# Performance work log

Measured on AMD Instinct MI355X. Metric: run time of the kernel, lower is better.

The kernel has to match this reference:

```python
import jax, jax.numpy as jnp
import numpy as np

NUM_HEADS = 16
D_MODEL = 1024
B, T = 2, 2048


def setup_inputs() -> dict:
    key = jax.random.key(0)
    ks = jax.random.split(key, 5)
    s = 1.0 / np.sqrt(D_MODEL)
    return {
        "x": jax.random.normal(ks[0], (B, T, D_MODEL), dtype=jnp.float32),
        "Wq": jax.random.normal(ks[1], (D_MODEL, D_MODEL), dtype=jnp.float32) * s,
        "Wk": jax.random.normal(ks[2], (D_MODEL, D_MODEL), dtype=jnp.float32) * s,
        "Wv": jax.random.normal(ks[3], (D_MODEL, D_MODEL), dtype=jnp.float32) * s,
        "Wo": jax.random.normal(ks[4], (D_MODEL, D_MODEL), dtype=jnp.float32) * s,
    }


def reference(x, Wq, Wk, Wv, Wo):
    # x: [B, T, D]; W*: [D, D] (torch nn.Linear weight layout, y = x @ W.T)
    b, t, d = x.shape
    h = NUM_HEADS
    hd = d // h

    def split_heads(y):
        # [B, T, D] -> [B, H, T, hd]
        return y.reshape(b, t, h, hd).transpose(0, 2, 1, 3)

    q = split_heads(x @ Wq.T)
    k = split_heads(x @ Wk.T)
    v = split_heads(x @ Wv.T)

    # scale uses last dim AFTER head split: 1/sqrt(head_dim)
    scores = jnp.einsum("bhqd,bhkd->bhqk", q, k) / jnp.sqrt(jnp.asarray(hd, x.dtype))
    causal = jnp.tril(jnp.ones((t, t), dtype=bool))  # [T, T]
    scores = jnp.where(causal[None, None], scores, -jnp.inf)
    attn = jax.nn.softmax(scores, axis=-1)  # [B, H, T, T]

    out = jnp.einsum("bhqk,bhkd->bhqd", attn, v)  # [B, H, T, hd]
    out = out.transpose(0, 2, 1, 3).reshape(b, t, d)  # concat heads
    return out @ Wo.T
```

## Files before the change

### kernel.cpp

```cpp
#include <hip/hip_runtime.h>
#include <hip/hip_bf16.h>

#define T_SEQ 2048
#define DM    1024
#define MTOT  4096

typedef short v8s __attribute__((ext_vector_type(8)));
typedef short v4s __attribute__((ext_vector_type(4)));
typedef float v4f __attribute__((ext_vector_type(4)));

__device__ __forceinline__ unsigned short f2bf(float f) {
  union { float f; unsigned int u; } x; x.f = f;
  return (unsigned short)((x.u + (((x.u >> 16) & 1u) + 0x7fffu)) >> 16);
}

__device__ __forceinline__ unsigned int pk2(float a, float b) {
  unsigned int ua = __float_as_uint(a) + 0x8000u;
  unsigned int ub = __float_as_uint(b) + 0x8000u;
  return __builtin_amdgcn_perm(ub, ua, 0x07060302u);
}

__device__ __forceinline__ v8s pack8bf(v4f a, v4f b) {
  union { v8s s; unsigned int u[4]; } o;
  o.u[0] = pk2(a[0], a[1]);
  o.u[1] = pk2(a[2], a[3]);
  o.u[2] = pk2(b[0], b[1]);
  o.u[3] = pk2(b[2], b[3]);
  return o.s;
}

__device__ __forceinline__ float fast_exp2(float x) {
#if __has_builtin(__builtin_amdgcn_exp2f)
  return __builtin_amdgcn_exp2f(x);
#else
  return exp2f(x);
#endif
}

__device__ __forceinline__ void gload16(const void* g, void* lds) {
  __builtin_amdgcn_global_load_lds(
      (const __attribute__((address_space(1))) unsigned int*)g,
      (__attribute__((address_space(3))) unsigned int*)lds, 16, 0, 0);
}

__global__ __launch_bounds__(256) void convert_all(
    const float* __restrict__ x,
    const float* __restrict__ Wq, const float* __restrict__ Wk,
    const float* __restrict__ Wv, const float* __restrict__ Wo,
    unsigned short* __restrict__ xb, unsigned short* __restrict__ wb)
{
  int i = blockIdx.x * 256 + threadIdx.x;
  const float4* src;
  ushort4* dst;
  int idx;
  if (i < (1 << 20)) {
    src = (const float4*)x; dst = (ushort4*)xb; idx = i;
  } else {
    int j = i - (1 << 20);
    int wsel = j >> 18;
    idx = j & ((1 << 18) - 1);
    const float* s = (wsel == 0) ? Wq : (wsel == 1) ? Wk : (wsel == 2) ? Wv : Wo;
    src = (const float4*)s;
    dst = (ushort4*)(wb + (size_t)wsel * DM * DM);
  }
  float4 v = src[idx];
  ushort4 o = { f2bf(v.x), f2bf(v.y), f2bf(v.z), f2bf(v.w) };
  dst[idx] = o;
}

__global__ __launch_bounds__(256) void qkv_fused2(
    const unsigned short* __restrict__ xb,
    const unsigned short* __restrict__ wb,
    unsigned short* __restrict__ Qw, unsigned short* __restrict__ Kw,
    unsigned short* __restrict__ Vtw)
{
  __shared__ unsigned short smem[20480];
  unsigned short* As = smem;

  const int tid  = threadIdx.x;
  const int wv   = tid >> 6, l = tid & 63;
  const int lrow = l & 15, lq = l >> 4;
  const int wm = wv >> 1;
  const int wn = wv & 1;
  const int srow = l >> 3, sslot = l & 7;
  const int swz  = sslot ^ (srow & 7);
  const int m0 = blockIdx.x * 128, n0 = blockIdx.y * 64;

  v4f acc[3][4][2];
#pragma unroll
  for (int z = 0; z < 3; ++z)
#pragma unroll
    for (int mt = 0; mt < 4; ++mt)
#pragma unroll
      for (int nt = 0; nt < 2; ++nt) acc[z][mt][nt] = (v4f){0.f, 0.f, 0.f, 0.f};

  const size_t aBase = (size_t)(m0 + wv * 32 + srow) * DM + swz * 8;
  const size_t bBase = (size_t)(n0 + wv * 16 + srow) * DM + swz * 8;

  for (int k0 = 0; k0 < DM; k0 += 64) {
    __syncthreads();
#pragma unroll
    for (int i = 0; i < 4; ++i)
      gload16(xb + aBase + (size_t)i * 8 * DM + k0, As + (wv * 32 + i * 8) * 64);
#pragma unroll
    for (int z = 0; z < 3; ++z)
#pragma unroll
      for (int i = 0; i < 2; ++i)
        gload16(wb + (size_t)z * DM * DM + bBase + (size_t)i * 8 * DM + k0,
                smem + 8192 + z * 4096 + (wv * 16 + i * 8) * 64);
    __syncthreads();
#pragma unroll
    for (int kc = 0; kc < 2; ++kc) {
      const int aslot = ((kc << 2) | lq) ^ (lrow & 7);
      v8s af[4];
#pragma unroll
      for (int mt = 0; mt < 4; ++mt)
        af[mt] = *(const v8s*)&As[(wm * 64 + mt * 16 + lrow) * 64 + aslot * 8];
#pragma unroll
      for (int z = 0; z < 3; ++z) {
        const unsigned short* Bz = smem + 8192 + z * 4096;
        v8s bf[2];
#pragma unroll
        for (int nt = 0; nt < 2; ++nt)
          bf[nt] = *(const v8s*)&Bz[(wn * 32 + nt * 16 + lrow) * 64 + aslot * 8];
#pragma unroll
        for (int mt = 0; mt < 4; ++mt)
#pragma unroll
          for (int nt = 0; nt < 2; ++nt)
            acc[z][mt][nt] = __builtin_amdgcn_mfma_f32_16x16x32_bf16(
                af[mt], bf[nt], acc[z][mt][nt], 0, 0, 0);
      }
    }
  }

#pragma unroll
  for (int z = 0; z < 2; ++z) {
    unsigned short* Y = z ? Kw : Qw;
#pragma unroll
    for (int mt = 0; mt < 4; ++mt)
#pragma unroll
      for (int nt = 0; nt < 2; ++nt)
#pragma unroll
        for (int r = 0; r < 4; ++r) {
          int row = m0 + wm * 64 + mt * 16 + lq * 4 + r;
          int col = n0 + wn * 32 + nt * 16 + lrow;
          Y[(size_t)row * DM + col] = f2bf(acc[z][mt][nt][r]);
        }
  }

  __syncthreads();
#pragma unroll
  for (int mt = 0; mt < 4; ++mt)
#pragma unroll
    for (int nt = 0; nt < 2; ++nt)
#pragma unroll
      for (int r = 0; r < 4; ++r) {
        int trow = wm * 64 + mt * 16 + lq * 4 + r;
        int col  = wn * 32 + nt * 16 + lrow;
        int slot = (col >> 3) ^ (trow & 7);
        smem[trow * 64 + slot * 8 + (col & 7)] = f2bf(acc[2][mt][nt][r]);
      }
  __syncthreads();
  {
    const int d = tid & 63;
    const int quarter = tid >> 6;
    const int bb = m0 >> 11;
    const int tblk = (m0 & 2047) >> 7;
    const int h = n0 >> 6;
    const int bh = bb * 16 + h;
    unsigned short* dst = Vtw + (((size_t)bh * 16 + tblk) * 64 + d) * 128;
    const int ch = d >> 3, e7 = d & 7;
#pragma unroll
    for (int jj = 0; jj < 4; ++jj) {
      unsigned short vals[8];
#pragma unroll
      for (int e = 0; e < 8; ++e) {
        int st = quarter * 32 + (e >> 2) * 16 + jj * 4 + (e & 3);
        vals[e] = smem[st * 64 + (ch ^ (st & 7)) * 8 + e7];
      }
      *(v8s*)(dst + (quarter * 4 + jj) * 8) = *(const v8s*)vals;
    }
  }
}

__global__ __launch_bounds__(256) void oproj_gemm2(
    const unsigned short* __restrict__ AO,
    const unsigned short* __restrict__ Wob,
    float* __restrict__ Y)
{
  __shared__ unsigned short smem[12288];
  unsigned short* As = smem;
  unsigned short* Bs = smem + 4096;

  const int tid  = threadIdx.x;
  const int wv   = tid >> 6, l = tid & 63;
  const int lrow = l & 15, lq = l >> 4;
  const int wm = wv >> 1;
  const int wn = wv & 1;
  const int srow = l >> 3, sslot = l & 7;
  const int swz  = sslot ^ (srow & 7);
  const int m0 = blockIdx.x * 64, n0 = blockIdx.y * 128;

  v4f acc[2][4];
#pragma unroll
  for (int mt = 0; mt < 2; ++mt)
#pragma unroll
    for (int nt = 0; nt < 4; ++nt) acc[mt][nt] = (v4f){0.f, 0.f, 0.f, 0.f};

  const size_t aBase = (size_t)(m0 + wv * 16 + srow) * DM + swz * 8;
  const size_t bBase = (size_t)(n0 + wv * 32 + srow) * DM + swz * 8;

  for (int k0 = 0; k0 < DM; k0 += 64) {
    __syncthreads();
#pragma unroll
    for (int i = 0; i < 2; ++i)
      gload16(AO + aBase + (size_t)i * 8 * DM + k0, As + (wv * 16 + i * 8) * 64);
#pragma unroll
    for (int i = 0; i < 4; ++i)
      gload16(Wob + bBase + (size_t)i * 8 * DM + k0, Bs + (wv * 32 + i * 8) * 64);
    __syncthreads();
#pragma unroll
    for (int kc = 0; kc < 2; ++kc) {
      const int aslot = ((kc << 2) | lq) ^ (lrow & 7);
      v8s af[2], bf[4];
#pragma unroll
      for (int mt = 0; mt < 2; ++mt)
        af[mt] = *(const v8s*)&As[(wm * 32 + mt * 16 + lrow) * 64 + aslot * 8];
#pragma unroll
      for (int nt = 0; nt < 4; ++nt)
        bf[nt] = *(const v8s*)&Bs[(wn * 64 + nt * 16 + lrow) * 64 + aslot * 8];
#pragma unroll
      for (int mt = 0; mt < 2; ++mt)
#pragma unroll
        for (int nt = 0; nt < 4; ++nt)
          acc[mt][nt] = __builtin_amdgcn_mfma_f32_16x16x32_bf16(
              af[mt], bf[nt], acc[mt][nt], 0, 0, 0);
    }
  }
#pragma unroll
  for (int mt = 0; mt < 2; ++mt)
#pragma unroll
    for (int nt = 0; nt < 4; ++nt)
#pragma unroll
      for (int r = 0; r < 4; ++r) {
        int row = m0 + wm * 32 + mt * 16 + lq * 4 + r;
        int col = n0 + wn * 64 + nt * 16 + lrow;
        Y[(size_t)row * DM + col] = acc[mt][nt][r];
      }
}

__global__ __launch_bounds__(256) void attn8(
    const unsigned short* __restrict__ Q,
    const unsigned short* __restrict__ K,
    const unsigned short* __restrict__ Vt,
    unsigned short* __restrict__ O)
{
  __shared__ unsigned short Ks[2][128 * 64];
  __shared__ unsigned short Vts[2][64 * 128];

  const int tid  = threadIdx.x;
  const int wave = tid >> 6;
  const int lane = tid & 63;
  const int lrow = lane & 15;
  const int lq   = lane >> 4;
  const int gid  = blockIdx.x;
  const int qt   = 31 - (gid >> 5);
  const int bh   = gid & 31;
  const int b = bh >> 4, h = bh & 15;

  union { v8s s; unsigned int u[4]; } ones;
  ones.u[0] = 0x3F803F80u; ones.u[1] = 0x3F803F80u;
  ones.u[2] = 0x3F803F80u; ones.u[3] = 0x3F803F80u;

  const int qrow = qt * 64 + wave * 16 + lrow;
  const unsigned short* qp = Q + ((size_t)(b * T_SEQ + qrow)) * DM + h * 64;
  v8s qf0 = *(const v8s*)(qp + lq * 8);
  v8s qf1 = *(const v8s*)(qp + 32 + lq * 8);

  v4f oacc[4];
#pragma unroll
  for (int dt = 0; dt < 4; ++dt) oacc[dt] = (v4f){0.f, 0.f, 0.f, 0.f};
  v4f sacc = {0.f, 0.f, 0.f, 0.f};

  const int n128 = (qt >> 1) + 1;

  const int kchunk = (lane & 7) ^ ((lane >> 3) & 7);
  const unsigned short* kg =
      K + ((size_t)(b * T_SEQ) + wave * 8 + (lane >> 3)) * DM + h * 64 + kchunk * 8;
  const int vd = wave * 4 + (lane >> 4);
  const int vslot = lane & 15;
  const int vchunk = (vslot & 8) | ((vslot & 7) ^ (vd & 7));
  const unsigned short* vg =
      Vt + ((size_t)bh * 1024 + vd) * 128 + vchunk * 8;

  const int slot0 = lq ^ (lrow & 7);
  const int slot1 = (4 + lq) ^ (lrow & 7);

#define STAGE(tt, buf) do {                                                   \
    unsigned short* kd_ = Ks[buf] + (wave * 8) * 64;                          \
    _Pragma("unroll")                                                         \
    for (int i_ = 0; i_ < 4; ++i_)                                            \
      gload16(kg + ((size_t)(tt) * 128 + i_ * 32) * DM, kd_ + i_ * 32 * 64);  \
    unsigned short* vd_ = Vts[buf] + (wave * 4) * 128;                        \
    _Pragma("unroll")                                                         \
    for (int i_ = 0; i_ < 4; ++i_)                                            \
      gload16(vg + (size_t)(tt) * 8192 + i_ * 2048, vd_ + i_ * 16 * 128);     \
  } while (0)

  STAGE(0, 0);
  __syncthreads();

  int cur = 0;
  for (int tt = 0; tt < n128; ++tt) {
    if (tt + 1 < n128) STAGE(tt + 1, cur ^ 1);

    const int kb = tt * 128;
    const unsigned short* Kss = Ks[cur];
    const unsigned short* Vss = Vts[cur];

    v4f s[8];
    __builtin_amdgcn_s_setprio(1);
#pragma unroll
    for (int nt = 0; nt < 8; ++nt) {
      v4f a = {0.f, 0.f, 0.f, 0.f};
      v8s k0 = *(const v8s*)&Kss[(nt * 16 + lrow) * 64 + slot0 * 8];
      a = __builtin_amdgcn_mfma_f32_16x16x32_bf16(k0, qf0, a, 0, 0, 0);
      v8s k1 = *(const v8s*)&Kss[(nt * 16 + lrow) * 64 + slot1 * 8];
      a = __builtin_amdgcn_mfma_f32_16x16x32_bf16(k1, qf1, a, 0, 0, 0);
      s[nt] = a;
    }
    __builtin_amdgcn_s_setprio(0);

    const bool needmask = (kb + 127 > qt * 64 + wave * 16);
    if (needmask) {
#pragma unroll
      for (int nt = 0; nt < 8; ++nt)
#pragma unroll
        for (int r = 0; r < 4; ++r) {
          float p = fast_exp2(fmaf(s[nt][r], 0.18033688f, -23.0831206f));
          if (kb + nt * 16 + lq * 4 + r > qt * 64 + wave * 16 + lrow) p = 0.f;
          s[nt][r] = p;
        }
    } else {
#pragma unroll
      for (int nt = 0; nt < 8; ++nt)
#pragma unroll
        for (int r = 0; r < 4; ++r)
          s[nt][r] = fast_exp2(fmaf(s[nt][r], 0.18033688f, -23.0831206f));
    }

    v8s pf[4];
#pragma unroll
    for (int kp = 0; kp < 4; ++kp) pf[kp] = pack8bf(s[2 * kp], s[2 * kp + 1]);

    __builtin_amdgcn_s_setprio(1);
#pragma unroll
    for (int kp = 0; kp < 4; ++kp) {
      sacc = __builtin_amdgcn_mfma_f32_16x16x32_bf16(ones.s, pf[kp], sacc, 0, 0, 0);
#pragma unroll
      for (int dt = 0; dt < 4; ++dt) {
        int ch = kp * 4 + lq;
        int slot = (ch & 8) | ((ch & 7) ^ (lrow & 7));
        v8s vv = *(const v8s*)&Vss[(dt * 16 + lrow) * 128 + slot * 8];
        oacc[dt] = __builtin_amdgcn_mfma_f32_16x16x32_bf16(
            vv, pf[kp], oacc[dt], 0, 0, 0);
      }
    }
    __builtin_amdgcn_s_setprio(0);

    if (tt + 1 < n128) {
      __syncthreads();
      cur ^= 1;
    }
  }
#undef STAGE

  const float rinv = 1.0f / sacc[0];

  const int token = qt * 64 + wave * 16 + lrow;
  unsigned short* op = O + ((size_t)(b * T_SEQ + token)) * DM + h * 64;
#pragma unroll
  for (int dt = 0; dt < 4; ++dt) {
    union { v4s s; unsigned int u[2]; } o;
    o.u[0] = pk2(oacc[dt][0] * rinv, oacc[dt][1] * rinv);
    o.u[1] = pk2(oacc[dt][2] * rinv, oacc[dt][3] * rinv);
    *(v4s*)(op + dt * 16 + lq * 4) = o.s;
  }
}

extern "C" void kernel_launch(void* const* d_in, const int* in_sizes, int n_in,
                              void* d_out, int out_size, void* d_ws, size_t ws_size,
                              hipStream_t stream) {
  const float* x  = (const float*)d_in[0];
  const float* Wq = (const float*)d_in[1];
  const float* Wk = (const float*)d_in[2];
  const float* Wv = (const float*)d_in[3];
  const float* Wo = (const float*)d_in[4];
  float* out = (float*)d_out;

  unsigned short* xb  = (unsigned short*)d_ws;
  unsigned short* wb  = xb + (size_t)MTOT * DM;
  unsigned short* Qw  = wb + (size_t)4 * DM * DM;
  unsigned short* Kw  = Qw + (size_t)MTOT * DM;
  unsigned short* Vtw = Kw + (size_t)MTOT * DM;
  unsigned short* AO  = xb;

  convert_all<<<8192, 256, 0, stream>>>(x, Wq, Wk, Wv, Wo, xb, wb);
  qkv_fused2<<<dim3(32, 16), 256, 0, stream>>>(xb, wb, Qw, Kw, Vtw);
  attn8<<<1024, 256, 0, stream>>>(Qw, Kw, Vtw, AO);
  oproj_gemm2<<<dim3(64, 8), 256, 0, stream>>>(AO, wb + (size_t)3 * DM * DM, out);
}
```

Before: 163.2 us.

## Process two query sub-tiles per wave in attention to reuse K/V fragments

The attention kernel now gives each block a 128-row query tile, and each wave handles two 16-row query groups that share the same K and V shared-memory reads. This halves the K/V loads and block count per query, cutting redundant LDS reads and global staging. The block order also changes so heavy diagonal tiles go first and light ones follow, balancing the causal workload. The cost is double the accumulator registers, which may lower occupancy, and coarser masking.

Result: slower. 170.0 us (+4.1%).

```diff
diff --git a/kernel.cpp b/kernel.cpp
--- a/kernel.cpp
+++ b/kernel.cpp
@@ -249,7 +249,7 @@
       }
 }
 
-__global__ __launch_bounds__(256) void attn8(
+__global__ __launch_bounds__(256) void attn9(
     const unsigned short* __restrict__ Q,
     const unsigned short* __restrict__ K,
     const unsigned short* __restrict__ Vt,
@@ -264,7 +264,8 @@
   const int lrow = lane & 15;
   const int lq   = lane >> 4;
   const int gid  = blockIdx.x;
-  const int qt   = 31 - (gid >> 5);
+  const int qsel = gid >> 5;
+  const int qt2  = (qsel < 8) ? (15 - qsel) : (qsel - 8);
   const int bh   = gid & 31;
   const int b = bh >> 4, h = bh & 15;
 
@@ -272,17 +273,23 @@
   ones.u[0] = 0x3F803F80u; ones.u[1] = 0x3F803F80u;
   ones.u[2] = 0x3F803F80u; ones.u[3] = 0x3F803F80u;
 
-  const int qrow = qt * 64 + wave * 16 + lrow;
-  const unsigned short* qp = Q + ((size_t)(b * T_SEQ + qrow)) * DM + h * 64;
-  v8s qf0 = *(const v8s*)(qp + lq * 8);
-  v8s qf1 = *(const v8s*)(qp + 32 + lq * 8);
-
-  v4f oacc[4];
-#pragma unroll
-  for (int dt = 0; dt < 4; ++dt) oacc[dt] = (v4f){0.f, 0.f, 0.f, 0.f};
-  v4f sacc = {0.f, 0.f, 0.f, 0.f};
-
-  const int n128 = (qt >> 1) + 1;
+  const int qbase = qt2 * 128 + wave * 32;
+  const unsigned short* qp = Q + ((size_t)(b * T_SEQ + qbase + lrow)) * DM + h * 64;
+  v8s qf00 = *(const v8s*)(qp + lq * 8);
+  v8s qf01 = *(const v8s*)(qp + 32 + lq * 8);
+  v8s qf10 = *(const v8s*)(qp + 16 * DM + lq * 8);
+  v8s qf11 = *(const v8s*)(qp + 16 * DM + 32 + lq * 8);
+
+  v4f oacc0[4], oacc1[4];
+#pragma unroll
+  for (int dt = 0; dt < 4; ++dt) {
+    oacc0[dt] = (v4f){0.f, 0.f, 0.f, 0.f};
+    oacc1[dt] = (v4f){0.f, 0.f, 0.f, 0.f};
+  }
+  v4f sacc0 = {0.f, 0.f, 0.f, 0.f};
+  v4f sacc1 = {0.f, 0.f, 0.f, 0.f};
+
+  const int n128 = qt2 + 1;
 
   const int kchunk = (lane & 7) ^ ((lane >> 3) & 7);
   const unsigned short* kg =
@@ -318,52 +325,72 @@
     const unsigned short* Kss = Ks[cur];
     const unsigned short* Vss = Vts[cur];
 
-    v4f s[8];
+    v4f s0[8], s1[8];
     __builtin_amdgcn_s_setprio(1);
 #pragma unroll
     for (int nt = 0; nt < 8; ++nt) {
-      v4f a = {0.f, 0.f, 0.f, 0.f};
       v8s k0 = *(const v8s*)&Kss[(nt * 16 + lrow) * 64 + slot0 * 8];
-      a = __builtin_amdgcn_mfma_f32_16x16x32_bf16(k0, qf0, a, 0, 0, 0);
       v8s k1 = *(const v8s*)&Kss[(nt * 16 + lrow) * 64 + slot1 * 8];
-      a = __builtin_amdgcn_mfma_f32_16x16x32_bf16(k1, qf1, a, 0, 0, 0);
-      s[nt] = a;
+      v4f a0 = {0.f, 0.f, 0.f, 0.f};
+      a0 = __builtin_amdgcn_mfma_f32_16x16x32_bf16(k0, qf00, a0, 0, 0, 0);
+      a0 = __builtin_amdgcn_mfma_f32_16x16x32_bf16(k1, qf01, a0, 0, 0, 0);
+      v4f a1 = {0.f, 0.f, 0.f, 0.f};
+      a1 = __builtin_amdgcn_mfma_f32_16x16x32_bf16(k0, qf10, a1, 0, 0, 0);
+      a1 = __builtin_amdgcn_mfma_f32_16x16x32_bf16(k1, qf11, a1, 0, 0, 0);
+      s0[nt] = a0;
+      s1[nt] = a1;
     }
     __builtin_amdgcn_s_setprio(0);
 
-    const bool needmask = (kb + 127 > qt * 64 + wave * 16);
-    if (needmask) {
+    const bool needmask0 = (kb + 127 > qbase);
+    if (needmask0) {
 #pragma unroll
       for (int nt = 0; nt < 8; ++nt)
 #pragma unroll
         for (int r = 0; r < 4; ++r) {
-          float p = fast_exp2(fmaf(s[nt][r], 0.18033688f, -23.0831206f));
-          if (kb + nt * 16 + lq * 4 + r > qt * 64 + wave * 16 + lrow) p = 0.f;
-          s[nt][r] = p;
+          float p = fast_exp2(fmaf(s0[nt][r], 0.18033688f, -23.0831206f));
+          if (kb + nt * 16 + lq * 4 + r > qbase + lrow) p = 0.f;
+          s0[nt][r] = p;
+        }
+#pragma unroll
+      for (int nt = 0; nt < 8; ++nt)
+#pragma unroll
+        for (int r = 0; r < 4; ++r) {
+          float p = fast_exp2(fmaf(s1[nt][r], 0.18033688f, -23.0831206f));
+          if (kb + nt * 16 + lq * 4 + r > qbase + 16 + lrow) p = 0.f;
+          s1[nt][r] = p;
         }
     } else {
 #pragma unroll
       for (int nt = 0; nt < 8; ++nt)
 #pragma unroll
-        for (int r = 0; r < 4; ++r)
-          s[nt][r] = fast_exp2(fmaf(s[nt][r], 0.18033688f, -23.0831206f));
-    }
-
-    v8s pf[4];
-#pragma unroll
-    for (int kp = 0; kp < 4; ++kp) pf[kp] = pack8bf(s[2 * kp], s[2 * kp + 1]);
+        for (int r = 0; r < 4; ++r) {
+          s0[nt][r] = fast_exp2(fmaf(s0[nt][r], 0.18033688f, -23.0831206f));
+          s1[nt][r] = fast_exp2(fmaf(s1[nt][r], 0.18033688f, -23.0831206f));
+        }
+    }
+
+    v8s pf0[4], pf1[4];
+#pragma unroll
+    for (int kp = 0; kp < 4; ++kp) {
+      pf0[kp] = pack8bf(s0[2 * kp], s0[2 * kp + 1]);
+      pf1[kp] = pack8bf(s1[2 * kp], s1[2 * kp + 1]);
+    }
 
     __builtin_amdgcn_s_setprio(1);
 #pragma unroll
     for (int kp = 0; kp < 4; ++kp) {
-      sacc = __builtin_amdgcn_mfma_f32_16x16x32_bf16(ones.s, pf[kp], sacc, 0, 0, 0);
+      sacc0 = __builtin_amdgcn_mfma_f32_16x16x32_bf16(ones.s, pf0[kp], sacc0, 0, 0, 0);
+      sacc1 = __builtin_amdgcn_mfma_f32_16x16x32_bf16(ones.s, pf1[kp], sacc1, 0, 0, 0);
 #pragma unroll
       for (int dt = 0; dt < 4; ++dt) {
         int ch = kp * 4 + lq;
         int slot = (ch & 8) | ((ch & 7) ^ (lrow & 7));
         v8s vv = *(const v8s*)&Vss[(dt * 16 + lrow) * 128 + slot * 8];
-        oacc[dt] = __builtin_amdgcn_mfma_f32_16x16x32_bf16(
-            vv, pf[kp], oacc[dt], 0, 0, 0);
+        oacc0[dt] = __builtin_amdgcn_mfma_f32_16x16x32_bf16(
+            vv, pf0[kp], oacc0[dt], 0, 0, 0);
+        oacc1[dt] = __builtin_amdgcn_mfma_f32_16x16x32_bf16(
+            vv, pf1[kp], oacc1[dt], 0, 0, 0);
       }
     }
     __builtin_amdgcn_s_setprio(0);
@@ -375,16 +402,21 @@
   }
 #undef STAGE
 
-  const float rinv = 1.0f / sacc[0];
-
-  const int token = qt * 64 + wave * 16 + lrow;
-  unsigned short* op = O + ((size_t)(b * T_SEQ + token)) * DM + h * 64;
+  const float rinv0 = 1.0f / sacc0[0];
+  const float rinv1 = 1.0f / sacc1[0];
+
+  unsigned short* op0 = O + ((size_t)(b * T_SEQ + qbase + lrow)) * DM + h * 64;
+  unsigned short* op1 = op0 + (size_t)16 * DM;
 #pragma unroll
   for (int dt = 0; dt < 4; ++dt) {
     union { v4s s; unsigned int u[2]; } o;
-    o.u[0] = pk2(oacc[dt][0] * rinv, oacc[dt][1] * rinv);
-    o.u[1] = pk2(oacc[dt][2] * rinv, oacc[dt][3] * rinv);
-    *(v4s*)(op + dt * 16 + lq * 4) = o.s;
+    o.u[0] = pk2(oacc0[dt][0] * rinv0, oacc0[dt][1] * rinv0);
+    o.u[1] = pk2(oacc0[dt][2] * rinv0, oacc0[dt][3] * rinv0);
+    *(v4s*)(op0 + dt * 16 + lq * 4) = o.s;
+    union { v4s s; unsigned int u[2]; } o1;
+    o1.u[0] = pk2(oacc1[dt][0] * rinv1, oacc1[dt][1] * rinv1);
+    o1.u[1] = pk2(oacc1[dt][2] * rinv1, oacc1[dt][3] * rinv1);
+    *(v4s*)(op1 + dt * 16 + lq * 4) = o1.s;
   }
 }
 
@@ -407,6 +439,6 @@
 
   convert_all<<<8192, 256, 0, stream>>>(x, Wq, Wk, Wv, Wo, xb, wb);
   qkv_fused2<<<dim3(32, 16), 256, 0, stream>>>(xb, wb, Qw, Kw, Vtw);
-  attn8<<<1024, 256, 0, stream>>>(Qw, Kw, Vtw, AO);
+  attn9<<<512, 256, 0, stream>>>(Qw, Kw, Vtw, AO);
   oproj_gemm2<<<dim3(64, 8), 256, 0, stream>>>(AO, wb + (size_t)3 * DM * DM, out);
 }
```

## Load K fragments directly from global memory and stage only V in LDS

Applied to the files above, without the earlier changes.

The attention kernel stops staging K tiles through shared memory. Each wave now reads its K MFMA fragments straight from global memory, so only V stays double-buffered in LDS, which roughly halves LDS use and adds launch bounds asking for 4 blocks per SM. The V prefetch now starts after the end-of-tile barrier, with an extra barrier before the PV stage. This trades LDS staging and reuse across waves for repeated global/L2 reads of K by all four waves, and less overlap of V loads with compute.

Result: slower. 213.7 us (+30.9%).

```diff
diff --git a/kernel.cpp b/kernel.cpp
--- a/kernel.cpp
+++ b/kernel.cpp
@@ -249,13 +249,12 @@
       }
 }
 
-__global__ __launch_bounds__(256) void attn8(
+__global__ __launch_bounds__(256, 4) void attn11(
     const unsigned short* __restrict__ Q,
     const unsigned short* __restrict__ K,
     const unsigned short* __restrict__ Vt,
     unsigned short* __restrict__ O)
 {
-  __shared__ unsigned short Ks[2][128 * 64];
   __shared__ unsigned short Vts[2][64 * 128];
 
   const int tid  = threadIdx.x;
@@ -284,48 +283,37 @@
 
   const int n128 = (qt >> 1) + 1;
 
-  const int kchunk = (lane & 7) ^ ((lane >> 3) & 7);
-  const unsigned short* kg =
-      K + ((size_t)(b * T_SEQ) + wave * 8 + (lane >> 3)) * DM + h * 64 + kchunk * 8;
+  const unsigned short* kgl =
+      K + ((size_t)(b * T_SEQ) + lrow) * DM + h * 64 + lq * 8;
+
   const int vd = wave * 4 + (lane >> 4);
   const int vslot = lane & 15;
   const int vchunk = (vslot & 8) | ((vslot & 7) ^ (vd & 7));
   const unsigned short* vg =
       Vt + ((size_t)bh * 1024 + vd) * 128 + vchunk * 8;
 
-  const int slot0 = lq ^ (lrow & 7);
-  const int slot1 = (4 + lq) ^ (lrow & 7);
-
-#define STAGE(tt, buf) do {                                                   \
-    unsigned short* kd_ = Ks[buf] + (wave * 8) * 64;                          \
-    _Pragma("unroll")                                                         \
-    for (int i_ = 0; i_ < 4; ++i_)                                            \
-      gload16(kg + ((size_t)(tt) * 128 + i_ * 32) * DM, kd_ + i_ * 32 * 64);  \
+#define STAGE_V(tt, buf) do {                                                 \
     unsigned short* vd_ = Vts[buf] + (wave * 4) * 128;                        \
     _Pragma("unroll")                                                         \
     for (int i_ = 0; i_ < 4; ++i_)                                            \
       gload16(vg + (size_t)(tt) * 8192 + i_ * 2048, vd_ + i_ * 16 * 128);     \
   } while (0)
 
-  STAGE(0, 0);
-  __syncthreads();
-
-  int cur = 0;
+  STAGE_V(0, 0);
+
   for (int tt = 0; tt < n128; ++tt) {
-    if (tt + 1 < n128) STAGE(tt + 1, cur ^ 1);
-
+    const int cur = tt & 1;
     const int kb = tt * 128;
-    const unsigned short* Kss = Ks[cur];
-    const unsigned short* Vss = Vts[cur];
 
     v4f s[8];
     __builtin_amdgcn_s_setprio(1);
 #pragma unroll
     for (int nt = 0; nt < 8; ++nt) {
+      const unsigned short* kr = kgl + (size_t)(kb + nt * 16) * DM;
       v4f a = {0.f, 0.f, 0.f, 0.f};
-      v8s k0 = *(const v8s*)&Kss[(nt * 16 + lrow) * 64 + slot0 * 8];
+      v8s k0 = *(const v8s*)(kr);
       a = __builtin_amdgcn_mfma_f32_16x16x32_bf16(k0, qf0, a, 0, 0, 0);
-      v8s k1 = *(const v8s*)&Kss[(nt * 16 + lrow) * 64 + slot1 * 8];
+      v8s k1 = *(const v8s*)(kr + 32);
       a = __builtin_amdgcn_mfma_f32_16x16x32_bf16(k1, qf1, a, 0, 0, 0);
       s[nt] = a;
     }
@@ -353,6 +341,8 @@
 #pragma unroll
     for (int kp = 0; kp < 4; ++kp) pf[kp] = pack8bf(s[2 * kp], s[2 * kp + 1]);
 
+    __syncthreads();
+
     __builtin_amdgcn_s_setprio(1);
 #pragma unroll
     for (int kp = 0; kp < 4; ++kp) {
@@ -361,7 +351,7 @@
       for (int dt = 0; dt < 4; ++dt) {
         int ch = kp * 4 + lq;
         int slot = (ch & 8) | ((ch & 7) ^ (lrow & 7));
-        v8s vv = *(const v8s*)&Vss[(dt * 16 + lrow) * 128 + slot * 8];
+        v8s vv = *(const v8s*)&Vts[cur][(dt * 16 + lrow) * 128 + slot * 8];
         oacc[dt] = __builtin_amdgcn_mfma_f32_16x16x32_bf16(
             vv, pf[kp], oacc[dt], 0, 0, 0);
       }
@@ -370,10 +360,10 @@
 
     if (tt + 1 < n128) {
       __syncthreads();
-      cur ^= 1;
-    }
-  }
-#undef STAGE
+      STAGE_V(tt + 1, cur ^ 1);
+    }
+  }
+#undef STAGE_V
 
   const float rinv = 1.0f / sacc[0];
 
@@ -407,6 +397,6 @@
 
   convert_all<<<8192, 256, 0, stream>>>(x, Wq, Wk, Wv, Wo, xb, wb);
   qkv_fused2<<<dim3(32, 16), 256, 0, stream>>>(xb, wb, Qw, Kw, Vtw);
-  attn8<<<1024, 256, 0, stream>>>(Qw, Kw, Vtw, AO);
+  attn11<<<1024, 256, 0, stream>>>(Qw, Kw, Vtw, AO);
   oproj_gemm2<<<dim3(64, 8), 256, 0, stream>>>(AO, wb + (size_t)3 * DM * DM, out);
 }
```
